# Optimization experiments

Measured on AMD Instinct MI355X. Metric: run time of the kernel, lower is better.

Reference implementation:

```python
import jax, jax.numpy as jnp
import numpy as np

B, S, D, HID, NH, R = 64, 2048, 512, 512, 8, 4
DH = D // NH
EPS = 1e-4


def setup_inputs() -> dict:
    key = jax.random.key(0)
    ks = jax.random.split(key, 32)
    w = lambda k, shape: 0.02 * jax.random.normal(k, shape, dtype=jnp.float32)
    embeddings = jax.random.normal(ks[0], (B, S, D), dtype=jnp.float32)
    attention_mask = jax.random.randint(ks[1], (B, S), 0, 2).astype(jnp.int32)
    attention_mask = attention_mask.at[:, 0].set(1)  # guarantee >=1 valid token
    return {
        'embeddings': embeddings,
        'attention_mask': attention_mask,
        # Theory-of-Mind pooled attention
        'Wk': w(ks[2], (D, D)), 'Wv': w(ks[3], (D, D)),
        'q_tom': w(ks[4], (NH, DH)), 'W_tom_fuse': w(ks[5], (D, D)),
        'w_hp': w(ks[6], (D, 1)), 'b_hp': jnp.zeros((1,), jnp.float32),
        # GCACU
        'Wg1': w(ks[7], (D, HID)), 'bg1': jnp.zeros((HID,), jnp.float32),
        'Wg2': w(ks[8], (HID, D)), 'bg2': jnp.zeros((D,), jnp.float32),
        'w_inc': w(ks[9], (D, 1)), 'b_inc': jnp.zeros((1,), jnp.float32),
        # CLoST head (setup/punchline means -> humor prob)
        'Wc1': w(ks[10], (2 * D, HID)), 'bc1': jnp.zeros((HID,), jnp.float32),
        'wc2': w(ks[11], (HID, 1)), 'bc2': jnp.zeros((1,), jnp.float32),
        # mHC low-rank stream mixing
        'U_mhc': w(ks[12], (3, R)), 'V_mhc': w(ks[13], (R, 3)),
        # SEVADE evaluator
        'Ws1': w(ks[14], (D + 3, HID)), 'bs1': jnp.zeros((HID,), jnp.float32),
        'ws2': w(ks[15], (HID, 1)), 'bs2': jnp.zeros((1,), jnp.float32),
        # final head
        'Wf1': w(ks[16], (D + 3, HID)), 'bf1': jnp.zeros((HID,), jnp.float32),
        'wf2': w(ks[17], (HID, 1)), 'bf2': jnp.zeros((1,), jnp.float32),
    }


def safe_logit(p, eps=EPS):
    p = jnp.clip(p, eps, 1.0 - eps)
    return jnp.log(p / (1.0 - p))


def _forward(embeddings, attention_mask, Wk, Wv, q_tom, W_tom_fuse, w_hp, b_hp,
             Wg1, bg1, Wg2, bg2, w_inc, b_inc, Wc1, bc1, wc2, bc2,
             U_mhc, V_mhc, Ws1, bs1, ws2, bs2, Wf1, bf1, wf2, bf2):
    x = embeddings  # [B,S,D]
    m = attention_mask.astype(x.dtype)  # [B,S]

    # --- ToM: learned-query pooled multi-head attention ---
    k = (x @ Wk).reshape(x.shape[0], x.shape[1], NH, DH)  # [B,S,H,dh]
    v = (x @ Wv).reshape(x.shape[0], x.shape[1], NH, DH)
    scores = jnp.einsum('hd,bshd->bhs', q_tom, k) / jnp.sqrt(jnp.float32(DH))
    scores = jnp.where(m[:, None, :] > 0, scores, -1e9)
    attn = jax.nn.softmax(scores, axis=-1)  # [B,H,S]
    fused = jnp.einsum('bhs,bshd->bhd', attn, v).reshape(x.shape[0], D)
    fused_mental = fused @ W_tom_fuse  # [B,D]
    tom_hp = jax.nn.sigmoid(fused_mental @ w_hp + b_hp)  # [B,1]

    # --- GCACU: masked mean -> MLP contextual stream + incongruity ---
    denom = jnp.sum(m, axis=1, keepdims=True)  # [B,1]
    mean_tok = jnp.sum(x * m[..., None], axis=1) / denom  # [B,D]
    ctx = jax.nn.relu(mean_tok @ Wg1 + bg1) @ Wg2 + bg2  # [B,D]
    inc = jax.nn.sigmoid(ctx @ w_inc + b_inc)  # [B,1]

    # --- CLoST: vectorized ragged setup/punchline split (torch code loops per sample) ---
    cum = jnp.cumsum(m, axis=1)  # rank of each valid token, [B,S]
    valid_count = cum[:, -1]  # [B]
    split = jnp.maximum(1, jnp.floor(valid_count * 0.6).astype(jnp.int32)).astype(x.dtype)
    setup_mask = m * (cum <= split[:, None])
    punch_mask = m * (cum > split[:, None])
    punch_cnt = jnp.sum(punch_mask, axis=1, keepdims=True)
    last_mask = m * (cum == valid_count[:, None])  # fallback: last valid token
    punch_mask = jnp.where(punch_cnt > 0, punch_mask, last_mask)
    setup_mean = jnp.sum(x * setup_mask[..., None], 1) / jnp.sum(setup_mask, 1)[:, None]
    punch_mean = jnp.sum(x * punch_mask[..., None], 1) / jnp.sum(punch_mask, 1)[:, None]
    h = jax.nn.relu(jnp.concatenate([setup_mean, punch_mean], -1) @ Wc1 + bc1)
    clost_prob = jax.nn.sigmoid(h @ wc2 + bc2)  # [B,1]
    clost_stream = 0.5 * (setup_mean + punch_mean)  # [B,D]

    scores3 = jnp.concatenate([tom_hp, inc, clost_prob], axis=1)  # [B,3]
    streams = jnp.stack([fused_mental, ctx, clost_stream], axis=1)  # [B,3,D]

    # --- mHC: residual low-rank stream mixing + manifold (unit-norm) constraint ---
    M = jnp.eye(3, dtype=x.dtype) + U_mhc @ V_mhc  # [3,3]
    mixed = jnp.einsum('st,btd->bsd', M, streams)
    mixed = mixed / (jnp.linalg.norm(mixed, axis=-1, keepdims=True) + 1e-6)

    # --- SEVADE evaluator ---
    sev_in = jnp.concatenate([mixed.mean(axis=1), scores3], axis=-1)
    sev_logits = jax.nn.relu(sev_in @ Ws1 + bs1) @ ws2 + bs2  # [B,1]

    # --- final head + logit fusion ---
    pooled = mixed.mean(axis=1)  # [B,D]
    fused_logits = jax.nn.relu(jnp.concatenate([pooled, scores3], -1) @ Wf1 + bf1) @ wf2 + bf2
    logits = fused_logits + 0.5 * sev_logits + 0.1 * safe_logit(scores3.mean(axis=1, keepdims=True))
    return logits  # [B,1]


def reference(embeddings, attention_mask, Wk, Wv, q_tom, W_tom_fuse, w_hp, b_hp,
              Wg1, bg1, Wg2, bg2, w_inc, b_inc, Wc1, bc1, wc2, bc2,
              U_mhc, V_mhc, Ws1, bs1, ws2, bs2, Wf1, bf1, wf2, bf2):
    return _forward(embeddings, attention_mask, Wk, Wv, q_tom, W_tom_fuse, w_hp, b_hp,
                    Wg1, bg1, Wg2, bg2, w_inc, b_inc, Wc1, bc1, wc2, bc2,
                    U_mhc, V_mhc, Ws1, bs1, ws2, bs2, Wf1, bf1, wf2, bf2)
```

## Files before the change

### kernel.cpp

```cpp
#include <hip/hip_runtime.h>
#include <math.h>

#define B_  64
#define S_  2048
#define D_  512
#define NH_ 8

static const size_t OFF_WKEFF  = 0;
static const size_t OFF_XPART  = 4096;
static const size_t OFF_LPART  = 5246976;
static const size_t OFF_XA     = 5255168;
static const size_t OFF_SSUM   = 5517312;
static const size_t OFF_PSUM   = 5550080;
static const size_t OFF_FUSED  = 5582848;
static const size_t OFF_FM     = 5615616;
static const size_t OFF_MEANT  = 5648384;
static const size_t OFF_CATSP  = 5681152;
static const size_t OFF_CLOST  = 5746688;
static const size_t OFF_G1     = 5779456;
static const size_t OFF_CTX    = 5812224;
static const size_t OFF_HC     = 5844992;
static const size_t OFF_S3     = 5877760;
static const size_t OFF_HEADIN = 5878016;
static const size_t OFF_HS     = 5911296;
static const size_t OFF_HF     = 5944064;
static const size_t OFF_MINFO  = 5976832;

__device__ __forceinline__ float wave_sum64(float v) {
#define DPP_STEP(ctrl, rm) \
    v += __int_as_float(__builtin_amdgcn_update_dpp(0, __float_as_int(v), (ctrl), (rm), 0xf, true))
    DPP_STEP(0x111, 0xf);
    DPP_STEP(0x112, 0xf);
    DPP_STEP(0x114, 0xf);
    DPP_STEP(0x118, 0xf);
    DPP_STEP(0x142, 0xa);
    DPP_STEP(0x143, 0xc);
#undef DPP_STEP
    return __int_as_float(__builtin_amdgcn_readlane(__float_as_int(v), 63));
}

__global__ __launch_bounds__(256) void k_prep(const float* __restrict__ Wk,
                                              const float* __restrict__ q,
                                              const int* __restrict__ mask,
                                              float* __restrict__ wkeff,
                                              int* __restrict__ minfo) {
    int bx = blockIdx.x, tid = threadIdx.x;
    if (bx < 16) {
        int idx = bx * 256 + tid;
        int h = idx >> 9, e = idx & 511;
        float s = 0.f;
        #pragma unroll 8
        for (int d = 0; d < 64; ++d) s = fmaf(Wk[e * 512 + h * 64 + d], q[h * 64 + d], s);
        wkeff[h * 512 + e] = s * 0.125f;
        return;
    }
    {
        int b = bx - 16;
        __shared__ int sh[256];
        int m8[8]; int cnt = 0; int s0 = tid * 8;
        #pragma unroll
        for (int i = 0; i < 8; ++i) { m8[i] = mask[b * S_ + s0 + i] > 0; cnt += m8[i]; }
        sh[tid] = cnt; __syncthreads();
        for (int off = 1; off < 256; off <<= 1) {
            int add = (tid >= off) ? sh[tid - off] : 0;
            __syncthreads();
            sh[tid] += add;
            __syncthreads();
        }
        int total  = sh[255];
        int before = sh[tid] - cnt;
        int split  = max(1, (int)floorf((float)total * 0.6f));
        int cum = before;
        #pragma unroll
        for (int i = 0; i < 8; ++i) {
            if (m8[i]) {
                cum++;
                if (cum == split) minfo[b * 8 + 2] = s0 + i;
                if (cum == total) minfo[b * 8 + 3] = s0 + i;
            }
        }
        if (tid == 0) { minfo[b * 8 + 0] = total; minfo[b * 8 + 1] = split; }
    }
}

__global__ __launch_bounds__(256, 4) void k_main(const float* __restrict__ x,
                                                 const int* __restrict__ mask,
                                                 const float* __restrict__ wkeff,
                                                 const int* __restrict__ minfo,
                                                 float* __restrict__ xpart,
                                                 float* __restrict__ lpart) {
    const int b = blockIdx.x, chunk = blockIdx.y;
    const int tid = threadIdx.x, hg = tid >> 6, lane = tid & 63;
    const int h0 = hg * 2;
    const int col0 = lane * 8;

    float wk0[8], wk1[8];
    #pragma unroll
    for (int i = 0; i < 8; ++i) {
        wk0[i] = wkeff[h0 * 512 + col0 + i];
        wk1[i] = wkeff[(h0 + 1) * 512 + col0 + i];
    }

    const int boundary = minfo[b * 8 + 2];
    const int sb = chunk * 128;
    const int* mb = mask + b * S_;
    unsigned long long bm0 = __ballot(mb[sb + lane] > 0);
    unsigned long long bm1 = __ballot(mb[sb + 64 + lane] > 0);

    float acc0[8], acc1[8], sacc[8], pacc[8];
    #pragma unroll
    for (int i = 0; i < 8; ++i) { acc0[i] = 0.f; acc1[i] = 0.f; sacc[i] = 0.f; pacc[i] = 0.f; }
    float l0 = 0.f, l1 = 0.f;

    const float* base = x + (size_t)b * (S_ * D_) + (size_t)sb * D_ + col0;
    float4 A0 = *(const float4*)(base);
    float4 A1 = *(const float4*)(base + 4);
    float4 B0 = *(const float4*)(base + D_);
    float4 B1 = *(const float4*)(base + D_ + 4);

    for (int t = 0; t < 128; t += 2) {
        float xa8[8] = {A0.x, A0.y, A0.z, A0.w, A1.x, A1.y, A1.z, A1.w};
        float xb8[8] = {B0.x, B0.y, B0.z, B0.w, B1.x, B1.y, B1.z, B1.w};
        if (t + 2 < 128) {
            const float* nb = base + (size_t)(t + 2) * D_;
            A0 = *(const float4*)(nb);
            A1 = *(const float4*)(nb + 4);
            B0 = *(const float4*)(nb + D_);
            B1 = *(const float4*)(nb + D_ + 4);
        }
        float s00 = xa8[0] * wk0[0], s01 = xa8[0] * wk1[0];
        float s10 = xb8[0] * wk0[0], s11 = xb8[0] * wk1[0];
        #pragma unroll
        for (int i = 1; i < 8; ++i) {
            s00 = fmaf(xa8[i], wk0[i], s00);
            s01 = fmaf(xa8[i], wk1[i], s01);
            s10 = fmaf(xb8[i], wk0[i], s10);
            s11 = fmaf(xb8[i], wk1[i], s11);
        }
        float f00 = wave_sum64(s00);
        float f01 = wave_sum64(s01);
        float f10 = wave_sum64(s10);
        float f11 = wave_sum64(s11);

        unsigned long long bsel = (t < 64) ? bm0 : bm1;
        bool mm0 = ((bsel >> (t & 63)) & 1ULL) != 0;
        bool mm1 = ((bsel >> ((t + 1) & 63)) & 1ULL) != 0;

        float w00 = mm0 ? __expf(f00) : 0.f;
        float w01 = mm0 ? __expf(f01) : 0.f;
        float w10 = mm1 ? __expf(f10) : 0.f;
        float w11 = mm1 ? __expf(f11) : 0.f;
        l0 += w00 + w10;
        l1 += w01 + w11;
        #pragma unroll
        for (int i = 0; i < 8; ++i) {
            acc0[i] = fmaf(w10, xb8[i], fmaf(w00, xa8[i], acc0[i]));
            acc1[i] = fmaf(w11, xb8[i], fmaf(w01, xa8[i], acc1[i]));
        }
        if (hg == 0) {
            int sg0 = sb + t, sg1 = sb + t + 1;
            float fs0 = (mm0 && sg0 <= boundary) ? 1.f : 0.f;
            float fp0 = (mm0 && sg0 >  boundary) ? 1.f : 0.f;
            float fs1 = (mm1 && sg1 <= boundary) ? 1.f : 0.f;
            float fp1 = (mm1 && sg1 >  boundary) ? 1.f : 0.f;
            #pragma unroll
            for (int i = 0; i < 8; ++i) {
                sacc[i] = fmaf(fs1, xb8[i], fmaf(fs0, xa8[i], sacc[i]));
                pacc[i] = fmaf(fp1, xb8[i], fmaf(fp0, xa8[i], pacc[i]));
            }
        }
    }

    float* pbase = xpart + ((size_t)(b * 16 + chunk) * 10) * 512;
    float* d0 = pbase + (size_t)h0 * 512 + col0;
    float* d1 = d0 + 512;
    ((float4*)d0)[0] = make_float4(acc0[0], acc0[1], acc0[2], acc0[3]);
    ((float4*)d0)[1] = make_float4(acc0[4], acc0[5], acc0[6], acc0[7]);
    ((float4*)d1)[0] = make_float4(acc1[0], acc1[1], acc1[2], acc1[3]);
    ((float4*)d1)[1] = make_float4(acc1[4], acc1[5], acc1[6], acc1[7]);
    if (hg == 0) {
        float* ds = pbase + 8 * 512 + col0;
        float* dp = pbase + 9 * 512 + col0;
        ((float4*)ds)[0] = make_float4(sacc[0], sacc[1], sacc[2], sacc[3]);
        ((float4*)ds)[1] = make_float4(sacc[4], sacc[5], sacc[6], sacc[7]);
        ((float4*)dp)[0] = make_float4(pacc[0], pacc[1], pacc[2], pacc[3]);
        ((float4*)dp)[1] = make_float4(pacc[4], pacc[5], pacc[6], pacc[7]);
    }
    if (lane == 0) {
        lpart[(b * 16 + chunk) * 8 + h0]     = l0;
        lpart[(b * 16 + chunk) * 8 + h0 + 1] = l1;
    }
}

__global__ __launch_bounds__(256) void k_xared(const float* __restrict__ part,
                                               float* __restrict__ xa,
                                               float* __restrict__ ssum,
                                               float* __restrict__ psum) {
    int b = blockIdx.x, r = blockIdx.y;
    int e = blockIdx.z * 256 + threadIdx.x;
    float s = 0.f;
    #pragma unroll
    for (int c = 0; c < 16; ++c)
        s += part[(((size_t)(b * 16 + c)) * 10 + r) * 512 + e];
    if (r < 8)       xa[((size_t)b * 8 + r) * 512 + e] = s;
    else if (r == 8) ssum[b * 512 + e] = s;
    else             psum[b * 512 + e] = s;
}

__global__ __launch_bounds__(256) void k_means(const float* __restrict__ x,
                                               const float* __restrict__ ssum,
                                               const float* __restrict__ psum,
                                               const int* __restrict__ minfo,
                                               float* __restrict__ meantok,
                                               float* __restrict__ catsp,
                                               float* __restrict__ clost) {
    int b = blockIdx.x;
    int e = blockIdx.y * 256 + threadIdx.x;
    int total = minfo[b * 8 + 0], split = minfo[b * 8 + 1], last = minfo[b * 8 + 3];
    int pcnt = total - split;
    float ssv = ssum[b * 512 + e], psv = psum[b * 512 + e];
    float mt = (ssv + psv) / (float)total;
    float sm = ssv / (float)split;
    float pm = (pcnt > 0) ? psv / (float)pcnt : x[((size_t)b * S_ + last) * D_ + e];
    meantok[b * 512 + e] = mt;
    catsp[b * 1024 + e] = sm;
    catsp[b * 1024 + 512 + e] = pm;
    clost[b * 512 + e] = 0.5f * (sm + pm);
}

__global__ __launch_bounds__(256) void k_gemv3(
    const float* lpart,
    const float* A0_, int lda0, const float* W0_, const float* bi0_, float* o0_, int K0, int r0, int hm0,
    const float* A1_, int lda1, const float* W1_, const float* bi1_, float* o1_, int K1, int r1, int hm1,
    const float* A2_, int lda2, const float* W2_, const float* bi2_, float* o2_, int K2, int r2, int hm2) {
    const float* A; const float* W; const float* bias; float* out;
    int lda, K, relu_, hm;
    int z = blockIdx.z;
    if (z == 0)      { A = A0_; lda = lda0; W = W0_; bias = bi0_; out = o0_; K = K0; relu_ = r0; hm = hm0; }
    else if (z == 1) { A = A1_; lda = lda1; W = W1_; bias = bi1_; out = o1_; K = K1; relu_ = r1; hm = hm1; }
    else             { A = A2_; lda = lda2; W = W2_; bias = bi2_; out = o2_; K = K2; relu_ = r2; hm = hm2; }

    int b = blockIdx.x, jg = blockIdx.y;
    int tid = threadIdx.x, jl = tid & 63, part = tid >> 6;
    int j = jg * 64 + jl;
    const float* a = hm ? (A + ((size_t)(b * 8 + jg)) * 512) : (A + (size_t)b * lda);
    float scale = 1.f;
    if (hm) {
        float lsum = 0.f;
        #pragma unroll
        for (int c = 0; c < 16; ++c) lsum += lpart[(b * 16 + c) * 8 + jg];
        scale = 1.f / lsum;
    }

    __shared__ float sha[1024];
    for (int e = tid; e < K; e += 256) sha[e] = a[e] * scale;
    __syncthreads();

    int Kq = (K + 3) >> 2;
    int e0 = part * Kq, e1 = min(K, e0 + Kq);
    float acc = 0.f;
    int e = e0;
    for (; e + 8 <= e1; e += 8) {
        #pragma unroll
        for (int u = 0; u < 8; ++u)
            acc = fmaf(sha[e + u], W[(size_t)(e + u) * 512 + j], acc);
    }
    for (; e < e1; ++e) acc = fmaf(sha[e], W[(size_t)e * 512 + j], acc);

    __shared__ float shr[256];
    shr[tid] = acc;
    __syncthreads();
    if (part == 0) {
        float s = shr[jl] + shr[jl + 64] + shr[jl + 128] + shr[jl + 192];
        if (bias) s += bias[j];
        if (relu_) s = fmaxf(s, 0.f);
        out[(size_t)b * 512 + j] = s;
    }
}

__global__ __launch_bounds__(256) void k_scalmix(const float* __restrict__ fm,
                                                 const float* __restrict__ ctx,
                                                 const float* __restrict__ hc,
                                                 const float* __restrict__ clost,
                                                 const float* __restrict__ w_hp,  const float* __restrict__ b_hp,
                                                 const float* __restrict__ w_inc, const float* __restrict__ b_inc,
                                                 const float* __restrict__ wc2,   const float* __restrict__ bc2,
                                                 const float* __restrict__ U,
                                                 const float* __restrict__ V,
                                                 float* __restrict__ s3,
                                                 float* __restrict__ headin) {
    int b = blockIdx.x, tid = threadIdx.x;
    float a0 = 0.f, a1 = 0.f, a2 = 0.f;
    for (int e = tid; e < 512; e += 256) {
        a0 = fmaf(fm[b * 512 + e],  w_hp[e],  a0);
        a1 = fmaf(ctx[b * 512 + e], w_inc[e], a1);
        a2 = fmaf(hc[b * 512 + e],  wc2[e],   a2);
    }
    __shared__ float r[3][256];
    r[0][tid] = a0; r[1][tid] = a1; r[2][tid] = a2;
    __syncthreads();
    for (int off = 128; off > 0; off >>= 1) {
        if (tid < off) {
            r[0][tid] += r[0][tid + off];
            r[1][tid] += r[1][tid + off];
            r[2][tid] += r[2][tid + off];
        }
        __syncthreads();
    }
    __shared__ float s3sh[3];
    if (tid == 0) {
        s3sh[0] = 1.f / (1.f + __expf(-(r[0][0] + b_hp[0])));
        s3sh[1] = 1.f / (1.f + __expf(-(r[1][0] + b_inc[0])));
        s3sh[2] = 1.f / (1.f + __expf(-(r[2][0] + bc2[0])));
        s3[b * 4 + 0] = s3sh[0];
        s3[b * 4 + 1] = s3sh[1];
        s3[b * 4 + 2] = s3sh[2];
    }
    __syncthreads();
    float M3[3][3];
    #pragma unroll
    for (int s = 0; s < 3; ++s)
        #pragma unroll
        for (int t = 0; t < 3; ++t) {
            float acc = (s == t) ? 1.f : 0.f;
            #pragma unroll
            for (int r4 = 0; r4 < 4; ++r4) acc = fmaf(U[s * 4 + r4], V[r4 * 3 + t], acc);
            M3[s][t] = acc;
        }
    float mx[3][2];
    #pragma unroll
    for (int kk = 0; kk < 2; ++kk) {
        int e = tid + kk * 256;
        float t0 = fm[b * 512 + e], t1 = ctx[b * 512 + e], t2 = clost[b * 512 + e];
        #pragma unroll
        for (int s = 0; s < 3; ++s) mx[s][kk] = M3[s][0] * t0 + M3[s][1] * t1 + M3[s][2] * t2;
    }
    #pragma unroll
    for (int s = 0; s < 3; ++s) r[s][tid] = mx[s][0] * mx[s][0] + mx[s][1] * mx[s][1];
    __syncthreads();
    for (int off = 128; off > 0; off >>= 1) {
        if (tid < off) {
            r[0][tid] += r[0][tid + off];
            r[1][tid] += r[1][tid + off];
            r[2][tid] += r[2][tid + off];
        }
        __syncthreads();
    }
    __shared__ float nrm[3];
    if (tid < 3) nrm[tid] = sqrtf(r[tid][0]) + 1e-6f;
    __syncthreads();
    #pragma unroll
    for (int kk = 0; kk < 2; ++kk) {
        int e = tid + kk * 256;
        float p = (mx[0][kk] / nrm[0] + mx[1][kk] / nrm[1] + mx[2][kk] / nrm[2]) * (1.f / 3.f);
        headin[b * 520 + e] = p;
    }
    if (tid < 3) headin[b * 520 + 512 + tid] = s3sh[tid];
}

__global__ __launch_bounds__(256) void k_logit(const float* __restrict__ hs,
                                               const float* __restrict__ hf,
                                               const float* __restrict__ ws2, const float* __restrict__ bs2,
                                               const float* __restrict__ wf2, const float* __restrict__ bf2,
                                               const float* __restrict__ s3,
                                               float* __restrict__ out) {
    int b = blockIdx.x, tid = threadIdx.x;
    float a = 0.f, c = 0.f;
    for (int e = tid; e < 512; e += 256) {
        a = fmaf(hs[b * 512 + e], ws2[e], a);
        c = fmaf(hf[b * 512 + e], wf2[e], c);
    }
    __shared__ float r[2][256];
    r[0][tid] = a; r[1][tid] = c;
    __syncthreads();
    for (int off = 128; off > 0; off >>= 1) {
        if (tid < off) { r[0][tid] += r[0][tid + off]; r[1][tid] += r[1][tid + off]; }
        __syncthreads();
    }
    if (tid == 0) {
        float sev = r[0][0] + bs2[0];
        float fl  = r[1][0] + bf2[0];
        float p = (s3[b * 4] + s3[b * 4 + 1] + s3[b * 4 + 2]) * (1.f / 3.f);
        p = fminf(fmaxf(p, 1e-4f), 1.f - 1e-4f);
        out[b] = fl + 0.5f * sev + 0.1f * logf(p / (1.f - p));
    }
}

extern "C" void kernel_launch(void* const* d_in, const int* in_sizes, int n_in,
                              void* d_out, int out_size, void* d_ws, size_t ws_size,
                              hipStream_t stream) {
    const float* x     = (const float*)d_in[0];
    const int*   mask  = (const int*)d_in[1];
    const float* Wk    = (const float*)d_in[2];
    const float* Wv    = (const float*)d_in[3];
    const float* q_tom = (const float*)d_in[4];
    const float* Wtf   = (const float*)d_in[5];
    const float* w_hp  = (const float*)d_in[6];
    const float* b_hp  = (const float*)d_in[7];
    const float* Wg1   = (const float*)d_in[8];
    const float* bg1   = (const float*)d_in[9];
    const float* Wg2   = (const float*)d_in[10];
    const float* bg2   = (const float*)d_in[11];
    const float* w_inc = (const float*)d_in[12];
    const float* b_inc = (const float*)d_in[13];
    const float* Wc1   = (const float*)d_in[14];
    const float* bc1   = (const float*)d_in[15];
    const float* wc2   = (const float*)d_in[16];
    const float* bc2   = (const float*)d_in[17];
    const float* U     = (const float*)d_in[18];
    const float* V     = (const float*)d_in[19];
    const float* Ws1   = (const float*)d_in[20];
    const float* bs1   = (const float*)d_in[21];
    const float* ws2   = (const float*)d_in[22];
    const float* bs2   = (const float*)d_in[23];
    const float* Wf1   = (const float*)d_in[24];
    const float* bf1   = (const float*)d_in[25];
    const float* wf2   = (const float*)d_in[26];
    const float* bf2   = (const float*)d_in[27];

    float* ws      = (float*)d_ws;
    float* wkeff   = ws + OFF_WKEFF;
    float* xpart   = ws + OFF_XPART;
    float* lpart   = ws + OFF_LPART;
    float* xa      = ws + OFF_XA;
    float* ssum    = ws + OFF_SSUM;
    float* psum    = ws + OFF_PSUM;
    float* fused   = ws + OFF_FUSED;
    float* fm      = ws + OFF_FM;
    float* meantok = ws + OFF_MEANT;
    float* catsp   = ws + OFF_CATSP;
    float* clost   = ws + OFF_CLOST;
    float* g1      = ws + OFF_G1;
    float* ctxb    = ws + OFF_CTX;
    float* hc      = ws + OFF_HC;
    float* s3      = ws + OFF_S3;
    float* headin  = ws + OFF_HEADIN;
    float* hsb     = ws + OFF_HS;
    float* hfb     = ws + OFF_HF;
    int*   minfo   = (int*)(ws + OFF_MINFO);
    float* out     = (float*)d_out;

    hipLaunchKernelGGL(k_prep,   dim3(80),        dim3(256), 0, stream, Wk, q_tom, mask, wkeff, minfo);
    hipLaunchKernelGGL(k_main,   dim3(64, 16),    dim3(256), 0, stream, x, mask, wkeff, minfo,
                       xpart, lpart);
    hipLaunchKernelGGL(k_xared,  dim3(64, 10, 2), dim3(256), 0, stream, xpart, xa, ssum, psum);
    hipLaunchKernelGGL(k_means,  dim3(64, 2),     dim3(256), 0, stream, x, ssum, psum, minfo,
                       meantok, catsp, clost);
    hipLaunchKernelGGL(k_gemv3,  dim3(64, 8, 3),  dim3(256), 0, stream, lpart,
                       xa, 0, Wv, (const float*)nullptr, fused, 512, 0, 1,
                       meantok, 512, Wg1, bg1, g1, 512, 1, 0,
                       catsp, 1024, Wc1, bc1, hc, 1024, 1, 0);
    hipLaunchKernelGGL(k_gemv3,  dim3(64, 8, 2),  dim3(256), 0, stream, lpart,
                       fused, 512, Wtf, (const float*)nullptr, fm, 512, 0, 0,
                       g1, 512, Wg2, bg2, ctxb, 512, 0, 0,
                       (const float*)nullptr, 0, (const float*)nullptr, (const float*)nullptr,
                       (float*)nullptr, 0, 0, 0);
    hipLaunchKernelGGL(k_scalmix, dim3(64),       dim3(256), 0, stream, fm, ctxb, hc, clost,
                       w_hp, b_hp, w_inc, b_inc, wc2, bc2, U, V, s3, headin);
    hipLaunchKernelGGL(k_gemv3,  dim3(64, 8, 2),  dim3(256), 0, stream, lpart,
                       headin, 520, Ws1, bs1, hsb, 515, 1, 0,
                       headin, 520, Wf1, bf1, hfb, 515, 1, 0,
                       (const float*)nullptr, 0, (const float*)nullptr, (const float*)nullptr,
                       (float*)nullptr, 0, 0, 0);
    hipLaunchKernelGGL(k_logit,  dim3(64),        dim3(256), 0, stream, hsb, hfb, ws2, bs2, wf2, bf2, s3, out);
}
```

Measured before the change: 494.2 us.

## Split k_main tokens across waves with all heads per wave, fuse means into reduction

Each wave in k_main now handles all 8 heads for a quarter of the chunk's tokens, instead of each wave covering 2 heads over all 128 tokens. Every x row is therefore loaded once per block rather than once per wave. Per-wave partials are combined through shared memory before a single write of the chunk partial. The k_means kernel is folded into k_xared, removing one launch and the ssum/psum round trip. The cost is much higher register pressure (64 accumulators plus 64 weights per thread, occupancy hint lowered to 2), 16 wave reductions per step, and a serialized shared-memory accumulation with syncs.

After: 506.0 us. +2.4%, slower.

```diff
diff --git a/kernel.cpp b/kernel.cpp
--- a/kernel.cpp
+++ b/kernel.cpp
@@ -10,8 +10,6 @@
 static const size_t OFF_XPART  = 4096;
 static const size_t OFF_LPART  = 5246976;
 static const size_t OFF_XA     = 5255168;
-static const size_t OFF_SSUM   = 5517312;
-static const size_t OFF_PSUM   = 5550080;
 static const size_t OFF_FUSED  = 5582848;
 static const size_t OFF_FM     = 5615616;
 static const size_t OFF_MEANT  = 5648384;
@@ -83,34 +81,35 @@
     }
 }
 
-__global__ __launch_bounds__(256, 4) void k_main(const float* __restrict__ x,
+__global__ __launch_bounds__(256, 2) void k_main(const float* __restrict__ x,
                                                  const int* __restrict__ mask,
                                                  const float* __restrict__ wkeff,
                                                  const int* __restrict__ minfo,
                                                  float* __restrict__ xpart,
                                                  float* __restrict__ lpart) {
     const int b = blockIdx.x, chunk = blockIdx.y;
-    const int tid = threadIdx.x, hg = tid >> 6, lane = tid & 63;
-    const int h0 = hg * 2;
+    const int tid = threadIdx.x, wave = tid >> 6, lane = tid & 63;
     const int col0 = lane * 8;
 
-    float wk0[8], wk1[8];
-    #pragma unroll
-    for (int i = 0; i < 8; ++i) {
-        wk0[i] = wkeff[h0 * 512 + col0 + i];
-        wk1[i] = wkeff[(h0 + 1) * 512 + col0 + i];
-    }
+    float wk[8][8];
+    #pragma unroll
+    for (int h = 0; h < 8; ++h)
+        #pragma unroll
+        for (int i = 0; i < 8; ++i) wk[h][i] = wkeff[h * 512 + col0 + i];
 
     const int boundary = minfo[b * 8 + 2];
-    const int sb = chunk * 128;
-    const int* mb = mask + b * S_;
-    unsigned long long bm0 = __ballot(mb[sb + lane] > 0);
-    unsigned long long bm1 = __ballot(mb[sb + 64 + lane] > 0);
-
-    float acc0[8], acc1[8], sacc[8], pacc[8];
-    #pragma unroll
-    for (int i = 0; i < 8; ++i) { acc0[i] = 0.f; acc1[i] = 0.f; sacc[i] = 0.f; pacc[i] = 0.f; }
-    float l0 = 0.f, l1 = 0.f;
+    const int sb = chunk * 128 + wave * 32;
+    unsigned long long bm = __ballot(mask[b * S_ + sb + (lane & 31)] > 0);
+
+    float acc[8][8], sacc[8], pacc[8], l[8];
+    #pragma unroll
+    for (int h = 0; h < 8; ++h) {
+        l[h] = 0.f;
+        #pragma unroll
+        for (int i = 0; i < 8; ++i) acc[h][i] = 0.f;
+    }
+    #pragma unroll
+    for (int i = 0; i < 8; ++i) { sacc[i] = 0.f; pacc[i] = 0.f; }
 
     const float* base = x + (size_t)b * (S_ * D_) + (size_t)sb * D_ + col0;
     float4 A0 = *(const float4*)(base);
@@ -118,114 +117,127 @@
     float4 B0 = *(const float4*)(base + D_);
     float4 B1 = *(const float4*)(base + D_ + 4);
 
-    for (int t = 0; t < 128; t += 2) {
+    for (int t = 0; t < 32; t += 2) {
         float xa8[8] = {A0.x, A0.y, A0.z, A0.w, A1.x, A1.y, A1.z, A1.w};
         float xb8[8] = {B0.x, B0.y, B0.z, B0.w, B1.x, B1.y, B1.z, B1.w};
-        if (t + 2 < 128) {
+        if (t + 2 < 32) {
             const float* nb = base + (size_t)(t + 2) * D_;
             A0 = *(const float4*)(nb);
             A1 = *(const float4*)(nb + 4);
             B0 = *(const float4*)(nb + D_);
             B1 = *(const float4*)(nb + D_ + 4);
         }
-        float s00 = xa8[0] * wk0[0], s01 = xa8[0] * wk1[0];
-        float s10 = xb8[0] * wk0[0], s11 = xb8[0] * wk1[0];
-        #pragma unroll
-        for (int i = 1; i < 8; ++i) {
-            s00 = fmaf(xa8[i], wk0[i], s00);
-            s01 = fmaf(xa8[i], wk1[i], s01);
-            s10 = fmaf(xb8[i], wk0[i], s10);
-            s11 = fmaf(xb8[i], wk1[i], s11);
-        }
-        float f00 = wave_sum64(s00);
-        float f01 = wave_sum64(s01);
-        float f10 = wave_sum64(s10);
-        float f11 = wave_sum64(s11);
-
-        unsigned long long bsel = (t < 64) ? bm0 : bm1;
-        bool mm0 = ((bsel >> (t & 63)) & 1ULL) != 0;
-        bool mm1 = ((bsel >> ((t + 1) & 63)) & 1ULL) != 0;
-
-        float w00 = mm0 ? __expf(f00) : 0.f;
-        float w01 = mm0 ? __expf(f01) : 0.f;
-        float w10 = mm1 ? __expf(f10) : 0.f;
-        float w11 = mm1 ? __expf(f11) : 0.f;
-        l0 += w00 + w10;
-        l1 += w01 + w11;
+        float s0[8], s1[8];
+        #pragma unroll
+        for (int h = 0; h < 8; ++h) {
+            float a = xa8[0] * wk[h][0];
+            float c = xb8[0] * wk[h][0];
+            #pragma unroll
+            for (int i = 1; i < 8; ++i) {
+                a = fmaf(xa8[i], wk[h][i], a);
+                c = fmaf(xb8[i], wk[h][i], c);
+            }
+            s0[h] = a; s1[h] = c;
+        }
+        #pragma unroll
+        for (int h = 0; h < 8; ++h) { s0[h] = wave_sum64(s0[h]); s1[h] = wave_sum64(s1[h]); }
+
+        bool m0 = ((bm >> t) & 1ULL) != 0;
+        bool m1 = ((bm >> (t + 1)) & 1ULL) != 0;
+        float w0[8], w1[8];
+        #pragma unroll
+        for (int h = 0; h < 8; ++h) {
+            w0[h] = m0 ? __expf(s0[h]) : 0.f;
+            w1[h] = m1 ? __expf(s1[h]) : 0.f;
+            l[h] += w0[h] + w1[h];
+        }
+        int sg0 = sb + t, sg1 = sb + t + 1;
+        float fs0 = (m0 && sg0 <= boundary) ? 1.f : 0.f;
+        float fp0 = (m0 && sg0 >  boundary) ? 1.f : 0.f;
+        float fs1 = (m1 && sg1 <= boundary) ? 1.f : 0.f;
+        float fp1 = (m1 && sg1 >  boundary) ? 1.f : 0.f;
         #pragma unroll
         for (int i = 0; i < 8; ++i) {
-            acc0[i] = fmaf(w10, xb8[i], fmaf(w00, xa8[i], acc0[i]));
-            acc1[i] = fmaf(w11, xb8[i], fmaf(w01, xa8[i], acc1[i]));
-        }
-        if (hg == 0) {
-            int sg0 = sb + t, sg1 = sb + t + 1;
-            float fs0 = (mm0 && sg0 <= boundary) ? 1.f : 0.f;
-            float fp0 = (mm0 && sg0 >  boundary) ? 1.f : 0.f;
-            float fs1 = (mm1 && sg1 <= boundary) ? 1.f : 0.f;
-            float fp1 = (mm1 && sg1 >  boundary) ? 1.f : 0.f;
             #pragma unroll
-            for (int i = 0; i < 8; ++i) {
-                sacc[i] = fmaf(fs1, xb8[i], fmaf(fs0, xa8[i], sacc[i]));
-                pacc[i] = fmaf(fp1, xb8[i], fmaf(fp0, xa8[i], pacc[i]));
+            for (int h = 0; h < 8; ++h)
+                acc[h][i] = fmaf(w1[h], xb8[i], fmaf(w0[h], xa8[i], acc[h][i]));
+            sacc[i] = fmaf(fs1, xb8[i], fmaf(fs0, xa8[i], sacc[i]));
+            pacc[i] = fmaf(fp1, xb8[i], fmaf(fp0, xa8[i], pacc[i]));
+        }
+    }
+
+    __shared__ float sh[5120];
+    __shared__ float shl[4][8];
+    if (lane == 0) {
+        #pragma unroll
+        for (int h = 0; h < 8; ++h) shl[wave][h] = l[h];
+    }
+    for (int w = 0; w < 4; ++w) {
+        if (wave == w) {
+            if (w == 0) {
+                #pragma unroll
+                for (int h = 0; h < 8; ++h)
+                    #pragma unroll
+                    for (int i = 0; i < 8; ++i) sh[h * 512 + col0 + i] = acc[h][i];
+                #pragma unroll
+                for (int i = 0; i < 8; ++i) {
+                    sh[8 * 512 + col0 + i] = sacc[i];
+                    sh[9 * 512 + col0 + i] = pacc[i];
+                }
+            } else {
+                #pragma unroll
+                for (int h = 0; h < 8; ++h)
+                    #pragma unroll
+                    for (int i = 0; i < 8; ++i) sh[h * 512 + col0 + i] += acc[h][i];
+                #pragma unroll
+                for (int i = 0; i < 8; ++i) {
+                    sh[8 * 512 + col0 + i] += sacc[i];
+                    sh[9 * 512 + col0 + i] += pacc[i];
+                }
             }
         }
-    }
-
-    float* pbase = xpart + ((size_t)(b * 16 + chunk) * 10) * 512;
-    float* d0 = pbase + (size_t)h0 * 512 + col0;
-    float* d1 = d0 + 512;
-    ((float4*)d0)[0] = make_float4(acc0[0], acc0[1], acc0[2], acc0[3]);
-    ((float4*)d0)[1] = make_float4(acc0[4], acc0[5], acc0[6], acc0[7]);
-    ((float4*)d1)[0] = make_float4(acc1[0], acc1[1], acc1[2], acc1[3]);
-    ((float4*)d1)[1] = make_float4(acc1[4], acc1[5], acc1[6], acc1[7]);
-    if (hg == 0) {
-        float* ds = pbase + 8 * 512 + col0;
-        float* dp = pbase + 9 * 512 + col0;
-        ((float4*)ds)[0] = make_float4(sacc[0], sacc[1], sacc[2], sacc[3]);
-        ((float4*)ds)[1] = make_float4(sacc[4], sacc[5], sacc[6], sacc[7]);
-        ((float4*)dp)[0] = make_float4(pacc[0], pacc[1], pacc[2], pacc[3]);
-        ((float4*)dp)[1] = make_float4(pacc[4], pacc[5], pacc[6], pacc[7]);
-    }
-    if (lane == 0) {
-        lpart[(b * 16 + chunk) * 8 + h0]     = l0;
-        lpart[(b * 16 + chunk) * 8 + h0 + 1] = l1;
-    }
+        __syncthreads();
+    }
+    float* dst = xpart + (size_t)(b * 16 + chunk) * 5120;
+    for (int j = tid; j < 5120; j += 256) dst[j] = sh[j];
+    if (tid < 8)
+        lpart[(b * 16 + chunk) * 8 + tid] =
+            shl[0][tid] + shl[1][tid] + shl[2][tid] + shl[3][tid];
 }
 
 __global__ __launch_bounds__(256) void k_xared(const float* __restrict__ part,
+                                               const int* __restrict__ minfo,
+                                               const float* __restrict__ x,
                                                float* __restrict__ xa,
-                                               float* __restrict__ ssum,
-                                               float* __restrict__ psum) {
-    int b = blockIdx.x, r = blockIdx.y;
-    int e = blockIdx.z * 256 + threadIdx.x;
-    float s = 0.f;
-    #pragma unroll
-    for (int c = 0; c < 16; ++c)
-        s += part[(((size_t)(b * 16 + c)) * 10 + r) * 512 + e];
-    if (r < 8)       xa[((size_t)b * 8 + r) * 512 + e] = s;
-    else if (r == 8) ssum[b * 512 + e] = s;
-    else             psum[b * 512 + e] = s;
-}
-
-__global__ __launch_bounds__(256) void k_means(const float* __restrict__ x,
-                                               const float* __restrict__ ssum,
-                                               const float* __restrict__ psum,
-                                               const int* __restrict__ minfo,
                                                float* __restrict__ meantok,
                                                float* __restrict__ catsp,
                                                float* __restrict__ clost) {
-    int b = blockIdx.x;
-    int e = blockIdx.y * 256 + threadIdx.x;
-    int total = minfo[b * 8 + 0], split = minfo[b * 8 + 1], last = minfo[b * 8 + 3];
-    int pcnt = total - split;
-    float ssv = ssum[b * 512 + e], psv = psum[b * 512 + e];
-    float mt = (ssv + psv) / (float)total;
-    float sm = ssv / (float)split;
-    float pm = (pcnt > 0) ? psv / (float)pcnt : x[((size_t)b * S_ + last) * D_ + e];
-    meantok[b * 512 + e] = mt;
-    catsp[b * 1024 + e] = sm;
-    catsp[b * 1024 + 512 + e] = pm;
-    clost[b * 512 + e] = 0.5f * (sm + pm);
+    int b = blockIdx.x, r = blockIdx.y;
+    int e = blockIdx.z * 256 + threadIdx.x;
+    if (r < 8) {
+        float s = 0.f;
+        #pragma unroll
+        for (int c = 0; c < 16; ++c)
+            s += part[(((size_t)(b * 16 + c)) * 10 + r) * 512 + e];
+        xa[((size_t)b * 8 + r) * 512 + e] = s;
+    } else {
+        float ss = 0.f, ps = 0.f;
+        #pragma unroll
+        for (int c = 0; c < 16; ++c) {
+            size_t pb = (((size_t)(b * 16 + c)) * 10 + 8) * 512 + e;
+            ss += part[pb];
+            ps += part[pb + 512];
+        }
+        int total = minfo[b * 8 + 0], split = minfo[b * 8 + 1], last = minfo[b * 8 + 3];
+        int pcnt = total - split;
+        float mt = (ss + ps) / (float)total;
+        float sm = ss / (float)split;
+        float pm = (pcnt > 0) ? ps / (float)pcnt : x[((size_t)b * S_ + last) * D_ + e];
+        meantok[b * 512 + e] = mt;
+        catsp[b * 1024 + e] = sm;
+        catsp[b * 1024 + 512 + e] = pm;
+        clost[b * 512 + e] = 0.5f * (sm + pm);
+    }
 }
 
 __global__ __launch_bounds__(256) void k_gemv3(
@@ -423,8 +435,6 @@
     float* xpart   = ws + OFF_XPART;
     float* lpart   = ws + OFF_LPART;
     float* xa      = ws + OFF_XA;
-    float* ssum    = ws + OFF_SSUM;
-    float* psum    = ws + OFF_PSUM;
     float* fused   = ws + OFF_FUSED;
     float* fm      = ws + OFF_FM;
     float* meantok = ws + OFF_MEANT;
@@ -443,9 +453,8 @@
     hipLaunchKernelGGL(k_prep,   dim3(80),        dim3(256), 0, stream, Wk, q_tom, mask, wkeff, minfo);
     hipLaunchKernelGGL(k_main,   dim3(64, 16),    dim3(256), 0, stream, x, mask, wkeff, minfo,
                        xpart, lpart);
-    hipLaunchKernelGGL(k_xared,  dim3(64, 10, 2), dim3(256), 0, stream, xpart, xa, ssum, psum);
-    hipLaunchKernelGGL(k_means,  dim3(64, 2),     dim3(256), 0, stream, x, ssum, psum, minfo,
-                       meantok, catsp, clost);
+    hipLaunchKernelGGL(k_xared,  dim3(64, 9, 2),  dim3(256), 0, stream, xpart, minfo, x,
+                       xa, meantok, catsp, clost);
     hipLaunchKernelGGL(k_gemv3,  dim3(64, 8, 3),  dim3(256), 0, stream, lpart,
                        xa, 0, Wv, (const float*)nullptr, fused, 512, 0, 1,
                        meantok, 512, Wg1, bg1, g1, 512, 1, 0,
```
